# Performance work log

Measured on AMD Instinct MI355X. Metric: run time of the kernel, lower is better.

The kernel has to match this reference:

```python
import jax, jax.numpy as jnp
import numpy as np

B, F, D, H = 16384, 10, 512, 8
DH = D // H
EPS = 1e-5


def setup_inputs() -> dict:
    key = jax.random.key(0)
    ks = jax.random.split(key, 12)
    s = 1.0 / np.sqrt(D)
    inp = {
        "x": jax.random.normal(ks[0], (B, F), dtype=jnp.float32),
        # per-feature Linear(1, D): weight (F, D), bias (F, D)
        "Wf": jax.random.normal(ks[1], (F, D), dtype=jnp.float32) * 1.0,
        "bf": jax.random.normal(ks[2], (F, D), dtype=jnp.float32) * 0.1,
        # MHA in/out projections (torch layout: out_features x in_features)
        "Wq": jax.random.normal(ks[3], (D, D), dtype=jnp.float32) * s,
        "Wk": jax.random.normal(ks[4], (D, D), dtype=jnp.float32) * s,
        "Wv": jax.random.normal(ks[5], (D, D), dtype=jnp.float32) * s,
        "bq": jax.random.normal(ks[6], (D,), dtype=jnp.float32) * 0.02,
        "bk": jax.random.normal(ks[7], (D,), dtype=jnp.float32) * 0.02,
        "bv": jax.random.normal(ks[8], (D,), dtype=jnp.float32) * 0.02,
        "Wo": jax.random.normal(ks[9], (D, D), dtype=jnp.float32) * s,
        "bo": jax.random.normal(ks[10], (D,), dtype=jnp.float32) * 0.02,
        "gamma": jnp.ones((D,), dtype=jnp.float32),
        "beta": jnp.zeros((D,), dtype=jnp.float32),
    }
    return inp


def reference(x, Wf, bf, Wq, Wk, Wv, bq, bk, bv, Wo, bo, gamma, beta):
    # Fused per-feature scalar Linear + ReLU: (B,F,1)*(F,D) + (F,D) -> (B,F,D)
    p = jax.nn.relu(x[:, :, None] * Wf[None] + bf[None])
    # Multi-head self-attention (q = k = v = p), torch Linear: y = x @ W.T + b
    def heads(t):  # (B,F,D) -> (B,H,F,DH)
        return t.reshape(B, F, H, DH).transpose(0, 2, 1, 3)
    q = heads(p @ Wq.T + bq)
    k = heads(p @ Wk.T + bk)
    v = heads(p @ Wv.T + bv)
    scores = jnp.einsum("bhqd,bhkd->bhqk", q, k) / jnp.sqrt(jnp.float32(DH))
    attn = jax.nn.softmax(scores, axis=-1)
    o = jnp.einsum("bhqk,bhkd->bhqd", attn, v)
    o = o.transpose(0, 2, 1, 3).reshape(B, F, D) @ Wo.T + bo
    # LayerNorm over last dim
    mu = jnp.mean(o, axis=-1, keepdims=True)
    var = jnp.mean(jnp.square(o - mu), axis=-1, keepdims=True)
    ln = (o - mu) * jax.lax.rsqrt(var + EPS) * gamma + beta
    # sum pool over the function/sequence axis
    return jnp.sum(ln, axis=1)  # (B, D)
```

## Files before the change

### kernel.cpp

```cpp
#include <hip/hip_runtime.h>
#include <stdint.h>


typedef __bf16 bf16;
typedef __bf16 bf16x8 __attribute__((ext_vector_type(8)));
typedef float f32x4 __attribute__((ext_vector_type(4)));

#define EPS 1e-5f

static constexpr size_t O_ELEMS   = (size_t)16384 * 10 * 512;
static constexpr size_t O_BYTES   = O_ELEMS * 2;
static constexpr size_t WQKV_BYTES = (size_t)8 * 192 * 512 * 2;

__device__ __forceinline__ void async_copy16(void* lds, const void* g) {
  __builtin_amdgcn_global_load_lds(
      (const __attribute__((address_space(1))) uint32_t*)g,
      (__attribute__((address_space(3))) uint32_t*)lds, 16, 0, 0);
}

__global__ __launch_bounds__(256) void pack_weights(
    const float* __restrict__ Wq, const float* __restrict__ Wk,
    const float* __restrict__ Wv, const float* __restrict__ Wo,
    bf16* __restrict__ wqkv, bf16* __restrict__ wob) {
  int idx = blockIdx.x * 256 + threadIdx.x;
#pragma unroll
  for (int u = 0; u < 4; ++u) {
    int i = idx + u * 262144;
    if (i < 786432) {
      int pr = i >> 9, k = i & 511;
      int h = pr / 192, w = pr - h * 192;
      int t = w >> 6, r = w & 63;
      const float* src = (t == 0) ? Wq : ((t == 1) ? Wk : Wv);
      wqkv[i] = (bf16)src[(h * 64 + r) * 512 + k];
    } else {
      int j = i - 786432;
      wob[j] = (bf16)Wo[j];
    }
  }
}

__global__ __launch_bounds__(512, 2) void kern_fused(
    const float* __restrict__ x, const float* __restrict__ Wf,
    const float* __restrict__ bfv, const bf16* __restrict__ wqkv,
    const float* __restrict__ bq, const float* __restrict__ bk,
    const float* __restrict__ bv, bf16* __restrict__ O,
    const bf16* __restrict__ wob, const float* __restrict__ bo,
    const float* __restrict__ gamma, const float* __restrict__ beta,
    float* __restrict__ out) {
  __shared__ __align__(16) char smem[153600];
  char* sA  = smem;
  char* sB0 = smem + 81920;
  char* sB1 = smem + 106496;
  char* sQK = smem + 131072;
  bf16* vbuf = (bf16*)sB1;
  float* scp = (float*)(sB1 + 10240);

  const int tid = threadIdx.x;
  const int wave = tid >> 6;
  const int lane = tid & 63;
  const int lm = lane & 15;
  const int lg = lane >> 4;
  const int wm = wave >> 2;
  const int wn = wave & 3;
  const int b0 = blockIdx.x * 8;
  const int lr = lane >> 3;
  const int kcg = (lane & 7) ^ lr;
  const int x7 = lm & 7;

#pragma unroll
  for (int jb = 0; jb < 3; ++jb) {
    int rb = wave + 8 * jb;
    async_copy16(sB0 + rb * 1024, wqkv + (size_t)(rb * 8 + lr) * 512 + kcg * 8);
  }

#pragma unroll
  for (int it = 0; it < 10; ++it) {
    int c = tid + it * 512;
    int s = c / 640, rem = c - s * 640;
    int r = rem >> 3, kcp = rem & 7;
    int kc = kcp ^ (r & 7);
    int k = s * 64 + kc * 8;
    int bl = r / 10, f = r - bl * 10;
    float xv = x[(b0 + bl) * 10 + f];
    const float* wf = Wf + f * 512 + k;
    const float* bp = bfv + f * 512 + k;
    bf16x8 pv;
#pragma unroll
    for (int j = 0; j < 8; ++j) pv[j] = (bf16)fmaxf(xv * wf[j] + bp[j], 0.f);
    *(bf16x8*)(sA + s * 10240 + r * 128 + kcp * 16) = pv;
  }
  __syncthreads();

  for (int h = 0; h < 8; ++h) {
    f32x4 acc[3][3];
#pragma unroll
    for (int i = 0; i < 3; ++i)
#pragma unroll
      for (int j = 0; j < 3; ++j) { f32x4 z = {0.f, 0.f, 0.f, 0.f}; acc[i][j] = z; }

    for (int s = 0; s < 8; ++s) {
      int t = h * 8 + s;
      char* bufC = (t & 1) ? sB1 : sB0;
      char* bufN = (t & 1) ? sB0 : sB1;
      if (t != 63) {
        int tn = t + 1;
        int h2 = tn >> 3, s2 = tn & 7;
        const bf16* srcb = wqkv + (size_t)h2 * 98304 + s2 * 64 + kcg * 8;
#pragma unroll
        for (int jb = 0; jb < 3; ++jb) {
          int rb = wave + 8 * jb;
          async_copy16(bufN + rb * 1024, srcb + (size_t)(rb * 8 + lr) * 512);
        }
        asm volatile("s_waitcnt vmcnt(3)" ::: "memory");
      } else {
        asm volatile("s_waitcnt vmcnt(0)" ::: "memory");
      }
      __builtin_amdgcn_sched_barrier(0);
      __builtin_amdgcn_s_barrier();
      __builtin_amdgcn_sched_barrier(0);
#pragma unroll
      for (int kk = 0; kk < 2; ++kk) {
        int ch = ((kk * 4 + lg) ^ x7) << 4;
        bf16x8 af[3], bfr[3];
#pragma unroll
        for (int mt = 0; mt < 3; ++mt)
          if (mt < 2 || wm == 0)
            af[mt] = *(const bf16x8*)(sA + s * 10240 + (wm * 48 + mt * 16 + lm) * 128 + ch);
#pragma unroll
        for (int nt = 0; nt < 3; ++nt)
          bfr[nt] = *(const bf16x8*)(bufC + (wn * 48 + nt * 16 + lm) * 128 + ch);
        __builtin_amdgcn_s_setprio(1);
#pragma unroll
        for (int mt = 0; mt < 3; ++mt)
          if (mt < 2 || wm == 0)
#pragma unroll
            for (int nt = 0; nt < 3; ++nt)
              acc[mt][nt] = __builtin_amdgcn_mfma_f32_16x16x32_bf16(af[mt], bfr[nt], acc[mt][nt], 0, 0, 0);
        __builtin_amdgcn_s_setprio(0);
      }
      asm volatile("s_waitcnt lgkmcnt(0)" ::: "memory");
      __builtin_amdgcn_sched_barrier(0);
      __builtin_amdgcn_s_barrier();
      __builtin_amdgcn_sched_barrier(0);
    }

    {
      float bias[3];
#pragma unroll
      for (int nt = 0; nt < 3; ++nt) {
        int col = wn * 48 + nt * 16 + lm;
        bias[nt] = (col < 64) ? bq[h * 64 + col]
                 : (col < 128) ? bk[h * 64 + col - 64]
                 : bv[h * 64 + col - 128];
      }
#pragma unroll
      for (int mt = 0; mt < 3; ++mt) {
        int rowb = wm * 48 + mt * 16 + lg * 4;
        if (rowb < 80) {
#pragma unroll
          for (int r = 0; r < 4; ++r) {
            int rw = rowb + r;
#pragma unroll
            for (int nt = 0; nt < 3; ++nt) {
              int col = wn * 48 + nt * 16 + lm;
              float val = acc[mt][nt][r] + bias[nt];
              if (col < 128)
                *(bf16*)(sQK + rw * 256 + (((col >> 3) ^ (rw & 7)) << 4) + (col & 7) * 2) = (bf16)val;
              else
                vbuf[rw * 64 + (col - 128)] = (bf16)val;
            }
          }
        }
      }
    }
    __syncthreads();

    {
      const int b = wave;
      f32x4 sv = {0.f, 0.f, 0.f, 0.f};
      const int rowa = b * 10 + lm;
      const int x7r = rowa & 7;
#pragma unroll
      for (int kk = 0; kk < 2; ++kk) {
        bf16x8 qf = *(const bf16x8*)(sQK + rowa * 256 + (((kk * 4 + lg) ^ x7r) << 4));
        bf16x8 kf = *(const bf16x8*)(sQK + rowa * 256 + (((8 + kk * 4 + lg) ^ x7r) << 4));
        sv = __builtin_amdgcn_mfma_f32_16x16x32_bf16(qf, kf, sv, 0, 0, 0);
      }
#pragma unroll
      for (int r = 0; r < 4; ++r) {
        float val = (lm < 10) ? sv[r] * 0.125f : -1e30f;
        float mx = val;
#pragma unroll
        for (int off = 1; off < 16; off <<= 1) mx = fmaxf(mx, __shfl_xor(mx, off));
        float e = __expf(val - mx);
        float ssum = e;
#pragma unroll
        for (int off = 1; off < 16; off <<= 1) ssum += __shfl_xor(ssum, off);
        int i = lg * 4 + r;
        if (i < 10 && lm < 12) scp[(b * 10 + i) * 12 + lm] = e / ssum;
      }
    }

    {
      const int b = wave;
      const int d = lane;
      float vv[10];
#pragma unroll
      for (int j = 0; j < 10; ++j) vv[j] = (float)vbuf[(b * 10 + j) * 64 + d];
      bf16* Ob = O + ((size_t)(b0 + b) * 10) * 512 + h * 64 + d;
#pragma unroll
      for (int i = 0; i < 10; ++i) {
        const float* ar = scp + (b * 10 + i) * 12;
        f32x4 a0 = *(const f32x4*)ar;
        f32x4 a1 = *(const f32x4*)(ar + 4);
        float o = a0[0] * vv[0] + a0[1] * vv[1] + a0[2] * vv[2] + a0[3] * vv[3]
                + a1[0] * vv[4] + a1[1] * vv[5] + a1[2] * vv[6] + a1[3] * vv[7]
                + ar[8] * vv[8] + ar[9] * vv[9];
        Ob[(size_t)i * 512] = (bf16)o;
      }
    }
    __syncthreads();
  }

  {
    char* Ab0 = smem;
    char* Ab1 = smem + 5120;
    char* Bb0 = smem + 10240;
    char* Bb1 = smem + 43008;
    float* partial = (float*)(smem + 145920);
    float* stats   = (float*)(smem + 148992);
    const char* Ob = (const char*)(O + (size_t)blockIdx.x * 80 * 512);
    const char* Wb = (const char*)wob;

    const int srow  = lane >> 2;
    const int sgran = (lane & 3) ^ ((lane >> 3) & 3);

    f32x4 acc[3][8];
#pragma unroll
    for (int i = 0; i < 3; ++i)
#pragma unroll
      for (int j = 0; j < 8; ++j) { f32x4 z = {0.f, 0.f, 0.f, 0.f}; acc[i][j] = z; }

#define STAGE2(AbN, BbN, s_)                                                     \
    {                                                                            \
      size_t co = (size_t)(s_) * 64 + sgran * 16;                                \
      _Pragma("unroll")                                                          \
      for (int j = 0; j < 4; ++j) {                                              \
        int R0 = (wave * 4 + j) * 16;                                            \
        async_copy16((BbN) + R0 * 64, Wb + (size_t)(R0 + srow) * 1024 + co);     \
      }                                                                          \
      if (wave < 5) {                                                            \
        int R0 = wave * 16;                                                      \
        async_copy16((AbN) + R0 * 64, Ob + (size_t)(R0 + srow) * 1024 + co);     \
      }                                                                          \
    }

    STAGE2(Ab0, Bb0, 0);

    for (int s = 0; s < 16; ++s) {
      char* AbC = (s & 1) ? Ab1 : Ab0;
      char* BbC = (s & 1) ? Bb1 : Bb0;
      char* AbN = (s & 1) ? Ab0 : Ab1;
      char* BbN = (s & 1) ? Bb0 : Bb1;
      if (s != 15) {
        STAGE2(AbN, BbN, s + 1);
        if (wave < 5) asm volatile("s_waitcnt vmcnt(5)" ::: "memory");
        else          asm volatile("s_waitcnt vmcnt(4)" ::: "memory");
      } else {
        asm volatile("s_waitcnt vmcnt(0)" ::: "memory");
      }
      __builtin_amdgcn_sched_barrier(0);
      __builtin_amdgcn_s_barrier();
      __builtin_amdgcn_sched_barrier(0);

      bf16x8 a2[3], b2[8];
#pragma unroll
      for (int mt = 0; mt < 3; ++mt)
        if (mt < 2 || wm == 0) {
          int m = wm * 48 + mt * 16 + lm;
          a2[mt] = *(const bf16x8*)(AbC + (m >> 1) * 128 + (m & 1) * 64 + (((lg ^ ((m >> 1) & 3))) << 4));
        }
#pragma unroll
      for (int nt = 0; nt < 8; ++nt) {
        int n = wn * 128 + nt * 16 + lm;
        b2[nt] = *(const bf16x8*)(BbC + (n >> 1) * 128 + (n & 1) * 64 + (((lg ^ ((n >> 1) & 3))) << 4));
      }
      __builtin_amdgcn_s_setprio(1);
#pragma unroll
      for (int mt = 0; mt < 3; ++mt)
        if (mt < 2 || wm == 0)
#pragma unroll
          for (int nt = 0; nt < 8; ++nt)
            acc[mt][nt] = __builtin_amdgcn_mfma_f32_16x16x32_bf16(a2[mt], b2[nt], acc[mt][nt], 0, 0, 0);
      __builtin_amdgcn_s_setprio(0);

      asm volatile("s_waitcnt lgkmcnt(0)" ::: "memory");
      __builtin_amdgcn_sched_barrier(0);
      __builtin_amdgcn_s_barrier();
      __builtin_amdgcn_sched_barrier(0);
    }

#pragma unroll
    for (int nt = 0; nt < 8; ++nt) {
      float bb = bo[wn * 128 + nt * 16 + lm];
#pragma unroll
      for (int mt = 0; mt < 3; ++mt)
#pragma unroll
        for (int r = 0; r < 4; ++r) acc[mt][nt][r] += bb;
    }

#pragma unroll
    for (int mt = 0; mt < 3; ++mt)
#pragma unroll
      for (int r = 0; r < 4; ++r) {
        float s1 = 0.f, s2 = 0.f;
#pragma unroll
        for (int nt = 0; nt < 8; ++nt) { float v = acc[mt][nt][r]; s1 += v; s2 += v * v; }
#pragma unroll
        for (int off = 1; off < 16; off <<= 1) {
          s1 += __shfl_xor(s1, off);
          s2 += __shfl_xor(s2, off);
        }
        if (lm == 0) {
          int row = wm * 48 + mt * 16 + lg * 4 + r;
          if (row < 80) {
            partial[(row * 4 + wn) * 2]     = s1;
            partial[(row * 4 + wn) * 2 + 1] = s2;
          }
        }
      }
    __syncthreads();
    if (tid < 80) {
      float s1 = 0.f, s2 = 0.f;
#pragma unroll
      for (int w = 0; w < 4; ++w) {
        s1 += partial[(tid * 4 + w) * 2];
        s2 += partial[(tid * 4 + w) * 2 + 1];
      }
      float mu = s1 * (1.f / 512.f);
      float var = s2 * (1.f / 512.f) - mu * mu;
      stats[tid * 2]     = mu;
      stats[tid * 2 + 1] = rsqrtf(var + EPS);
    }
    __syncthreads();
    bf16* lnb = (bf16*)smem;
#pragma unroll
    for (int mt = 0; mt < 3; ++mt)
#pragma unroll
      for (int r = 0; r < 4; ++r) {
        int row = wm * 48 + mt * 16 + lg * 4 + r;
        if (row < 80) {
          float mu = stats[row * 2], rr = stats[row * 2 + 1];
#pragma unroll
          for (int nt = 0; nt < 8; ++nt) {
            int col = wn * 128 + nt * 16 + lm;
            lnb[row * 520 + col] = (bf16)((acc[mt][nt][r] - mu) * rr);
          }
        }
      }
    __syncthreads();
#pragma unroll
    for (int u = 0; u < 8; ++u) {
      int id = tid + u * 512;
      int b = id >> 9, n = id & 511;
      float ssum = 0.f;
#pragma unroll
      for (int f = 0; f < 10; ++f) ssum += (float)lnb[(b * 10 + f) * 520 + n];
      out[((size_t)blockIdx.x * 8 + b) * 512 + n] = gamma[n] * ssum + 10.f * beta[n];
    }
  }
#undef STAGE2
}

extern "C" void kernel_launch(void* const* d_in, const int* in_sizes, int n_in,
                              void* d_out, int out_size, void* d_ws, size_t ws_size,
                              hipStream_t stream) {
  const float* x     = (const float*)d_in[0];
  const float* Wf    = (const float*)d_in[1];
  const float* bfv   = (const float*)d_in[2];
  const float* Wq    = (const float*)d_in[3];
  const float* Wk    = (const float*)d_in[4];
  const float* Wv    = (const float*)d_in[5];
  const float* bq    = (const float*)d_in[6];
  const float* bk    = (const float*)d_in[7];
  const float* bv    = (const float*)d_in[8];
  const float* Wo    = (const float*)d_in[9];
  const float* bo    = (const float*)d_in[10];
  const float* gamma = (const float*)d_in[11];
  const float* beta  = (const float*)d_in[12];
  float* out = (float*)d_out;

  char* ws = (char*)d_ws;
  bf16* O    = (bf16*)ws;
  bf16* wqkv = (bf16*)(ws + O_BYTES);
  bf16* wob  = (bf16*)(ws + O_BYTES + WQKV_BYTES);

  pack_weights<<<1024, 256, 0, stream>>>(Wq, Wk, Wv, Wo, wqkv, wob);
  kern_fused<<<2048, 512, 0, stream>>>(x, Wf, bfv, wqkv, bq, bk, bv, O,
                                       wob, bo, gamma, beta, out);
}
```

Baseline: 709.2 us.

## Load QKV weight fragments directly into registers instead of LDS double buffer

The QKV projection's B operand used to be staged into a double-buffered LDS tile with async global-to-LDS copies and two block barriers per k-step. Now each lane loads its weight fragments straight from global memory into a register double buffer, prefetching one step ahead, and the k-loop is fully unrolled. This removes the per-step barriers and LDS traffic, shrinks shared memory, and moves one __syncthreads to sit before the per-head epilogue. In exchange, waves that share a weight tile each fetch it separately through the cache, and the extra fragment registers add pressure.

```diff
diff --git a/kernel.cpp b/kernel.cpp
--- a/kernel.cpp
+++ b/kernel.cpp
@@ -47,13 +47,11 @@
     const bf16* __restrict__ wob, const float* __restrict__ bo,
     const float* __restrict__ gamma, const float* __restrict__ beta,
     float* __restrict__ out) {
-  __shared__ __align__(16) char smem[153600];
+  __shared__ __align__(16) char smem[118528];
   char* sA  = smem;
-  char* sB0 = smem + 81920;
-  char* sB1 = smem + 106496;
-  char* sQK = smem + 131072;
-  bf16* vbuf = (bf16*)sB1;
-  float* scp = (float*)(sB1 + 10240);
+  char* sQK = smem + 81920;
+  bf16* vbuf = (bf16*)(smem + 104448);
+  float* scp = (float*)(smem + 114688);
 
   const int tid = threadIdx.x;
   const int wave = tid >> 6;
@@ -68,12 +66,6 @@
   const int x7 = lm & 7;
 
 #pragma unroll
-  for (int jb = 0; jb < 3; ++jb) {
-    int rb = wave + 8 * jb;
-    async_copy16(sB0 + rb * 1024, wqkv + (size_t)(rb * 8 + lr) * 512 + kcg * 8);
-  }
-
-#pragma unroll
   for (int it = 0; it < 10; ++it) {
     int c = tid + it * 512;
     int s = c / 640, rem = c - s * 640;
@@ -91,6 +83,15 @@
   }
   __syncthreads();
 
+  const bf16* wBlane = wqkv + (size_t)(wn * 48 + lm) * 512 + lg * 8;
+
+  bf16x8 b0f[3][2], b1f[3][2];
+#pragma unroll
+  for (int nt = 0; nt < 3; ++nt)
+#pragma unroll
+    for (int kk = 0; kk < 2; ++kk)
+      b0f[nt][kk] = *(const bf16x8*)(wBlane + nt * 8192 + kk * 32);
+
   for (int h = 0; h < 8; ++h) {
     f32x4 acc[3][3];
 #pragma unroll
@@ -98,51 +99,40 @@
 #pragma unroll
       for (int j = 0; j < 3; ++j) { f32x4 z = {0.f, 0.f, 0.f, 0.f}; acc[i][j] = z; }
 
+#pragma unroll
     for (int s = 0; s < 8; ++s) {
-      int t = h * 8 + s;
-      char* bufC = (t & 1) ? sB1 : sB0;
-      char* bufN = (t & 1) ? sB0 : sB1;
-      if (t != 63) {
-        int tn = t + 1;
-        int h2 = tn >> 3, s2 = tn & 7;
-        const bf16* srcb = wqkv + (size_t)h2 * 98304 + s2 * 64 + kcg * 8;
-#pragma unroll
-        for (int jb = 0; jb < 3; ++jb) {
-          int rb = wave + 8 * jb;
-          async_copy16(bufN + rb * 1024, srcb + (size_t)(rb * 8 + lr) * 512);
-        }
-        asm volatile("s_waitcnt vmcnt(3)" ::: "memory");
-      } else {
-        asm volatile("s_waitcnt vmcnt(0)" ::: "memory");
-      }
-      __builtin_amdgcn_sched_barrier(0);
-      __builtin_amdgcn_s_barrier();
-      __builtin_amdgcn_sched_barrier(0);
+      const int t = h * 8 + s;
+      bf16x8 (*bc)[2] = (s & 1) ? b1f : b0f;
+      bf16x8 (*bn)[2] = (s & 1) ? b0f : b1f;
+      if (t < 63) {
+        const int tn = t + 1;
+        const bf16* p = wBlane + (size_t)(tn >> 3) * 98304 + (tn & 7) * 64;
+#pragma unroll
+        for (int nt = 0; nt < 3; ++nt)
+#pragma unroll
+          for (int kk = 0; kk < 2; ++kk)
+            bn[nt][kk] = *(const bf16x8*)(p + nt * 8192 + kk * 32);
+      }
 #pragma unroll
       for (int kk = 0; kk < 2; ++kk) {
         int ch = ((kk * 4 + lg) ^ x7) << 4;
-        bf16x8 af[3], bfr[3];
+        bf16x8 af[3];
 #pragma unroll
         for (int mt = 0; mt < 3; ++mt)
           if (mt < 2 || wm == 0)
             af[mt] = *(const bf16x8*)(sA + s * 10240 + (wm * 48 + mt * 16 + lm) * 128 + ch);
-#pragma unroll
-        for (int nt = 0; nt < 3; ++nt)
-          bfr[nt] = *(const bf16x8*)(bufC + (wn * 48 + nt * 16 + lm) * 128 + ch);
         __builtin_amdgcn_s_setprio(1);
 #pragma unroll
         for (int mt = 0; mt < 3; ++mt)
           if (mt < 2 || wm == 0)
 #pragma unroll
             for (int nt = 0; nt < 3; ++nt)
-              acc[mt][nt] = __builtin_amdgcn_mfma_f32_16x16x32_bf16(af[mt], bfr[nt], acc[mt][nt], 0, 0, 0);
+              acc[mt][nt] = __builtin_amdgcn_mfma_f32_16x16x32_bf16(af[mt], bc[nt][kk], acc[mt][nt], 0, 0, 0);
         __builtin_amdgcn_s_setprio(0);
       }
-      asm volatile("s_waitcnt lgkmcnt(0)" ::: "memory");
-      __builtin_amdgcn_sched_barrier(0);
-      __builtin_amdgcn_s_barrier();
-      __builtin_amdgcn_sched_barrier(0);
-    }
+    }
+
+    __syncthreads();
 
     {
       float bias[3];
@@ -219,7 +209,6 @@
         Ob[(size_t)i * 512] = (bf16)o;
       }
     }
-    __syncthreads();
   }
 
   {
@@ -227,8 +216,8 @@
     char* Ab1 = smem + 5120;
     char* Bb0 = smem + 10240;
     char* Bb1 = smem + 43008;
-    float* partial = (float*)(smem + 145920);
-    float* stats   = (float*)(smem + 148992);
+    float* partial = (float*)(smem + 83200);
+    float* stats   = (float*)(smem + 85760);
     const char* Ob = (const char*)(O + (size_t)blockIdx.x * 80 * 512);
     const char* Wb = (const char*)wob;
 
```

After: 1.147 ms. 1.62x slower.
